# Kernel tuning notes

Measured on AMD Instinct MI355X. Metric: run time of the kernel, lower is better.

The kernel has to match this reference:

```python
import jax, jax.numpy as jnp
import numpy as np

B, L, C, D = 4, 128, 1024, 512

def setup_inputs() -> dict:
    key = jax.random.key(0)
    ks = jax.random.split(key, 6)
    scale = 1.0 / np.sqrt(D)
    return {
        "hidden": jax.random.normal(ks[0], (B, L, D), dtype=jnp.float32),
        "ctx": jax.random.normal(ks[1], (B, C, D), dtype=jnp.float32),
        "W": jax.random.normal(ks[2], (D, D), dtype=jnp.float32) * scale,
        "U": jax.random.normal(ks[3], (D, D), dtype=jnp.float32) * scale,
        "U_b": jax.random.normal(ks[4], (D,), dtype=jnp.float32) * scale,
        "V": jax.random.normal(ks[5], (D,), dtype=jnp.float32) * scale,
    }

def reference(hidden, ctx, W, U, U_b, V):
    # Bahdanau additive attention: softmax_j V . tanh(W h_i + U c_j + b)
    wq = jnp.einsum('bld,ed->ble', hidden, W)          # [B, L, D]
    uc = jnp.einsum('bcd,ed->bce', ctx, U) + U_b       # [B, C, D]
    s = jnp.tanh(wq[:, :, None, :] + uc[:, None, :, :])  # [B, L, C, D]
    align = jnp.einsum('blcd,d->blc', s, V)            # [B, L, C]
    return jax.nn.softmax(align, axis=-1)
```

## Files before the change

### kernel.cpp

```cpp
#include <hip/hip_runtime.h>
#include <hip/hip_bf16.h>


#define SCALE2 2.8853900817779268f

typedef _Float16 f16x8 __attribute__((ext_vector_type(8)));
typedef float f32x4 __attribute__((ext_vector_type(4)));

__device__ __forceinline__ void gload16(const void* g, void* l) {
    __builtin_amdgcn_global_load_lds(
        (const __attribute__((address_space(1))) void*)g,
        (__attribute__((address_space(3))) void*)l,
        16, 0, 0);
}

__global__ __launch_bounds__(256) void gemm_mfma(
    const float* __restrict__ hidden, const float* __restrict__ ctx,
    const float* __restrict__ Wmat, const float* __restrict__ Umat,
    const float* __restrict__ U_b,
    float* __restrict__ ewq_t, float* __restrict__ euc_t)
{
    __shared__ __align__(16) _Float16 Xh[2][64][40];
    __shared__ __align__(16) _Float16 Xl[2][64][40];
    __shared__ __align__(16) _Float16 Wh[2][64][40];
    __shared__ __align__(16) _Float16 Wl[2][64][40];

    const int tid  = threadIdx.x;
    const int lane = tid & 63;
    const int w    = tid >> 6;

    const float *X, *Wm, *bias;
    float* Ct;
    int m0, crow0, Mb, bshift;
    {
        int gb = blockIdx.x;
        if (gb < 64) {
            m0 = (gb & 7) * 64; crow0 = (gb >> 3) * 64;
            X = hidden; Wm = Wmat; bias = nullptr; Ct = ewq_t; Mb = 128; bshift = 7;
        } else {
            int g = gb - 64;
            m0 = (g & 7) * 64; crow0 = (g >> 3) * 64;
            X = ctx; Wm = Umat; bias = U_b; Ct = euc_t; Mb = 1024; bshift = 10;
        }
    }

    const int sr = tid >> 2;
    const int sk = (tid & 3) * 8;
    const float* xsrc = X  + (size_t)(crow0 + sr) * 512 + sk;
    const float* wsrc = Wm + (size_t)(m0    + sr) * 512 + sk;

    f32x4 acc[4];
#pragma unroll
    for (int t = 0; t < 4; ++t) acc[t] = (f32x4){0.f, 0.f, 0.f, 0.f};

    float xr[8], wr[8];
    {
        float4 a = *(const float4*)(xsrc);
        float4 b = *(const float4*)(xsrc + 4);
        float4 c = *(const float4*)(wsrc);
        float4 d = *(const float4*)(wsrc + 4);
        xr[0]=a.x; xr[1]=a.y; xr[2]=a.z; xr[3]=a.w; xr[4]=b.x; xr[5]=b.y; xr[6]=b.z; xr[7]=b.w;
        wr[0]=c.x; wr[1]=c.y; wr[2]=c.z; wr[3]=c.w; wr[4]=d.x; wr[5]=d.y; wr[6]=d.z; wr[7]=d.w;
        f16x8 xh, xl, wh, wl;
#pragma unroll
        for (int i = 0; i < 8; ++i) {
            xh[i] = (_Float16)xr[i]; xl[i] = (_Float16)(xr[i] - (float)xh[i]);
            wh[i] = (_Float16)wr[i]; wl[i] = (_Float16)(wr[i] - (float)wh[i]);
        }
        *(f16x8*)&Xh[0][sr][sk] = xh; *(f16x8*)&Xl[0][sr][sk] = xl;
        *(f16x8*)&Wh[0][sr][sk] = wh; *(f16x8*)&Wl[0][sr][sk] = wl;
    }

    const int fr = lane & 15;
    const int fk = (lane >> 4) * 8;
    const int mrow = w * 16 + fr;

    for (int kc = 0; kc < 16; ++kc) {
        if (kc < 15) {
            float4 a = *(const float4*)(xsrc + (kc + 1) * 32);
            float4 b = *(const float4*)(xsrc + (kc + 1) * 32 + 4);
            float4 c = *(const float4*)(wsrc + (kc + 1) * 32);
            float4 d = *(const float4*)(wsrc + (kc + 1) * 32 + 4);
            xr[0]=a.x; xr[1]=a.y; xr[2]=a.z; xr[3]=a.w; xr[4]=b.x; xr[5]=b.y; xr[6]=b.z; xr[7]=b.w;
            wr[0]=c.x; wr[1]=c.y; wr[2]=c.z; wr[3]=c.w; wr[4]=d.x; wr[5]=d.y; wr[6]=d.z; wr[7]=d.w;
        }
        __syncthreads();
        const int bu = kc & 1;
        const f16x8 ah = *(const f16x8*)&Wh[bu][mrow][fk];
        const f16x8 al = *(const f16x8*)&Wl[bu][mrow][fk];
#pragma unroll
        for (int t = 0; t < 4; ++t) {
            const f16x8 bh = *(const f16x8*)&Xh[bu][t * 16 + fr][fk];
            const f16x8 bl = *(const f16x8*)&Xl[bu][t * 16 + fr][fk];
            acc[t] = __builtin_amdgcn_mfma_f32_16x16x32_f16(ah, bh, acc[t], 0, 0, 0);
            acc[t] = __builtin_amdgcn_mfma_f32_16x16x32_f16(ah, bl, acc[t], 0, 0, 0);
            acc[t] = __builtin_amdgcn_mfma_f32_16x16x32_f16(al, bh, acc[t], 0, 0, 0);
        }
        if (kc < 15) {
            f16x8 xh, xl, wh, wl;
#pragma unroll
            for (int i = 0; i < 8; ++i) {
                xh[i] = (_Float16)xr[i]; xl[i] = (_Float16)(xr[i] - (float)xh[i]);
                wh[i] = (_Float16)wr[i]; wl[i] = (_Float16)(wr[i] - (float)wh[i]);
            }
            *(f16x8*)&Xh[bu ^ 1][sr][sk] = xh; *(f16x8*)&Xl[bu ^ 1][sr][sk] = xl;
            *(f16x8*)&Wh[bu ^ 1][sr][sk] = wh; *(f16x8*)&Wl[bu ^ 1][sr][sk] = wl;
        }
    }

    const int rbase = m0 + w * 16 + (lane >> 4) * 4;
    float bl4[4] = {0.f, 0.f, 0.f, 0.f};
    if (bias) {
        float4 t = *(const float4*)&bias[rbase];
        bl4[0] = t.x; bl4[1] = t.y; bl4[2] = t.z; bl4[3] = t.w;
    }
    const int bidx = crow0 >> bshift;
    const int cl0  = crow0 & (Mb - 1);
    float* obase = Ct + ((size_t)bidx * 512 + rbase) * Mb + cl0 + fr;
#pragma unroll
    for (int r = 0; r < 4; ++r)
#pragma unroll
        for (int t = 0; t < 4; ++t)
            obase[(size_t)r * Mb + t * 16] =
                __builtin_amdgcn_exp2f(SCALE2 * (acc[t][r] + bl4[r]));
}

__global__ __launch_bounds__(256) void fused_align9(
    const float* __restrict__ ewq_t,
    const float* __restrict__ euc_t,
    const float* __restrict__ Vv,
    float* __restrict__ p0, float* __restrict__ p1,
    float* __restrict__ p2, float* __restrict__ p3)
{
    __shared__ __align__(16) float uc_s[2][16][256];
    __shared__ __align__(16) float wq_s[2][16][16];
    __shared__ __align__(8)  float2 v2_s[64];

    const int tid  = threadIdx.x;
    const int lane = tid & 63;
    const int w    = __builtin_amdgcn_readfirstlane(tid >> 6);
    const int c0   = blockIdx.x * 256;
    const int l0   = blockIdx.y * 16;
    const int z    = blockIdx.z;
    const int b    = z >> 2, h = z & 3;
    const int d0   = h * 128;

    const float* ucb = euc_t + ((size_t)b * 512 + d0) * 1024 + c0;
    const float* wqb = ewq_t + ((size_t)b * 512 + d0) * 128 + l0;

    if (tid < 64)
        v2_s[tid] = make_float2(Vv[d0 + 2 * tid], Vv[d0 + 2 * tid + 1]);

#define STAGE(buf, chunk)                                                     \
    {                                                                         \
        _Pragma("unroll")                                                     \
        for (int i_ = 0; i_ < 4; ++i_) {                                      \
            const int d_ = w * 4 + i_;                                        \
            gload16(ucb + (size_t)((chunk) * 16 + d_) * 1024 + lane * 4,      \
                    &uc_s[buf][d_][0]);                                       \
        }                                                                     \
        if (w == 0)                                                           \
            gload16(wqb + (size_t)((chunk) * 16 + (lane >> 2)) * 128 +        \
                        (lane & 3) * 4,                                       \
                    &wq_s[buf][0][0]);                                        \
    }

    float acc[4][4];
#pragma unroll
    for (int i = 0; i < 4; ++i)
#pragma unroll
        for (int k = 0; k < 4; ++k) acc[i][k] = 0.0f;

    STAGE(0, 0);
    __syncthreads();

    for (int ch = 0; ch < 8; ++ch) {
        if (ch < 7) STAGE((ch + 1) & 1, ch + 1);
        const int bu = ch & 1;
#pragma unroll
        for (int j = 0; j < 8; ++j) {
            const float4 e0 = *(const float4*)&uc_s[bu][2 * j][lane * 4];
            const float4 e1 = *(const float4*)&uc_s[bu][2 * j + 1][lane * 4];
            const float4 q0 = *(const float4*)&wq_s[bu][2 * j][w * 4];
            const float4 q1 = *(const float4*)&wq_s[bu][2 * j + 1][w * 4];
            const float2 vp = v2_s[ch * 8 + j];
            const float q0a[4] = {q0.x, q0.y, q0.z, q0.w};
            const float q1a[4] = {q1.x, q1.y, q1.z, q1.w};
            const float e0a[4] = {e0.x, e0.y, e0.z, e0.w};
            const float e1a[4] = {e1.x, e1.y, e1.z, e1.w};
#pragma unroll
            for (int i = 0; i < 4; ++i) {
#pragma unroll
                for (int k = 0; k < 4; ++k) {
                    const float t0 = fmaf(q0a[i], e0a[k], 1.0f);
                    const float t1 = fmaf(q1a[i], e1a[k], 1.0f);
                    const float n  = fmaf(vp.x, t1, vp.y * t0);
                    acc[i][k] = fmaf(n, __builtin_amdgcn_rcpf(t0 * t1), acc[i][k]);
                }
            }
        }
        __syncthreads();
    }
#undef STAGE

    float* pp = (h == 0) ? p0 : (h == 1) ? p1 : (h == 2) ? p2 : p3;
#pragma unroll
    for (int i = 0; i < 4; ++i) {
        float4 r;
        r.x = -2.0f * acc[i][0]; r.y = -2.0f * acc[i][1];
        r.z = -2.0f * acc[i][2]; r.w = -2.0f * acc[i][3];
        *(float4*)(pp + ((size_t)b * 128 + l0 + w * 4 + i) * 1024 + c0 + lane * 4) = r;
    }
}

__global__ __launch_bounds__(256) void softmax3(
    float* __restrict__ data, const float* __restrict__ p1,
    const float* __restrict__ p2, const float* __restrict__ p3)
{
    const int row  = blockIdx.x * 4 + (threadIdx.x >> 6);
    const int lane = threadIdx.x & 63;
    float* p = data + (size_t)row * 1024;
    const float* q1 = p1 + (size_t)row * 1024;
    const float* q2 = p2 + (size_t)row * 1024;
    const float* q3 = p3 + (size_t)row * 1024;

    float4 x[4];
#pragma unroll
    for (int j = 0; j < 4; ++j) {
        float4 a = *(const float4*)(p  + j * 256 + lane * 4);
        float4 b = *(const float4*)(q1 + j * 256 + lane * 4);
        float4 c = *(const float4*)(q2 + j * 256 + lane * 4);
        float4 d = *(const float4*)(q3 + j * 256 + lane * 4);
        x[j].x = (a.x + b.x) + (c.x + d.x);
        x[j].y = (a.y + b.y) + (c.y + d.y);
        x[j].z = (a.z + b.z) + (c.z + d.z);
        x[j].w = (a.w + b.w) + (c.w + d.w);
    }

    float m = x[0].x;
#pragma unroll
    for (int j = 0; j < 4; ++j) {
        m = fmaxf(m, x[j].x); m = fmaxf(m, x[j].y);
        m = fmaxf(m, x[j].z); m = fmaxf(m, x[j].w);
    }
#pragma unroll
    for (int mask = 32; mask >= 1; mask >>= 1) m = fmaxf(m, __shfl_xor(m, mask, 64));

    const float LOG2E = 1.4426950408889634f;
    float s = 0.0f;
#pragma unroll
    for (int j = 0; j < 4; ++j) {
        x[j].x = __builtin_amdgcn_exp2f((x[j].x - m) * LOG2E);
        x[j].y = __builtin_amdgcn_exp2f((x[j].y - m) * LOG2E);
        x[j].z = __builtin_amdgcn_exp2f((x[j].z - m) * LOG2E);
        x[j].w = __builtin_amdgcn_exp2f((x[j].w - m) * LOG2E);
        s += x[j].x + x[j].y + x[j].z + x[j].w;
    }
#pragma unroll
    for (int mask = 32; mask >= 1; mask >>= 1) s += __shfl_xor(s, mask, 64);
    const float r = __builtin_amdgcn_rcpf(s);
#pragma unroll
    for (int j = 0; j < 4; ++j) {
        x[j].x *= r; x[j].y *= r; x[j].z *= r; x[j].w *= r;
        *(float4*)(p + j * 256 + lane * 4) = x[j];
    }
}

extern "C" void kernel_launch(void* const* d_in, const int* in_sizes, int n_in,
                              void* d_out, int out_size, void* d_ws, size_t ws_size,
                              hipStream_t stream)
{
    const float* hidden = (const float*)d_in[0];
    const float* ctx    = (const float*)d_in[1];
    const float* W      = (const float*)d_in[2];
    const float* U      = (const float*)d_in[3];
    const float* U_b    = (const float*)d_in[4];
    const float* V      = (const float*)d_in[5];
    float* out = (float*)d_out;

    float* ewq_t = (float*)d_ws;
    float* euc_t = ewq_t + 4 * 512 * 128;
    float* p1    = euc_t + 4 * 512 * 1024;
    float* p2    = p1 + 4 * 128 * 1024;
    float* p3    = p2 + 4 * 128 * 1024;

    gemm_mfma<<<576, 256, 0, stream>>>(hidden, ctx, W, U, U_b, ewq_t, euc_t);
    fused_align9<<<dim3(4, 8, 16), 256, 0, stream>>>(ewq_t, euc_t, V, out, p1, p2, p3);
    softmax3<<<128, 256, 0, stream>>>(out, p1, p2, p3);
}
```

Measured before the change: 54.27 us.

## Combine 16 rational terms into one fraction per chunk and split D into eight slices

Result: faster. 51.81 us (-4.5%).

```diff
diff --git a/kernel.cpp b/kernel.cpp
--- a/kernel.cpp
+++ b/kernel.cpp
@@ -3,6 +3,7 @@
 
 
 #define SCALE2 2.8853900817779268f
+#define PART (4 * 128 * 1024)
 
 typedef _Float16 f16x8 __attribute__((ext_vector_type(8)));
 typedef float f32x4 __attribute__((ext_vector_type(4)));
@@ -125,16 +126,15 @@
                 __builtin_amdgcn_exp2f(SCALE2 * (acc[t][r] + bl4[r]));
 }
 
-__global__ __launch_bounds__(256) void fused_align9(
+__global__ __launch_bounds__(256) void fused_align10(
     const float* __restrict__ ewq_t,
     const float* __restrict__ euc_t,
     const float* __restrict__ Vv,
-    float* __restrict__ p0, float* __restrict__ p1,
-    float* __restrict__ p2, float* __restrict__ p3)
+    float* __restrict__ pout, float* __restrict__ pws)
 {
     __shared__ __align__(16) float uc_s[2][16][256];
     __shared__ __align__(16) float wq_s[2][16][16];
-    __shared__ __align__(8)  float2 v2_s[64];
+    __shared__ float v_s[64];
 
     const int tid  = threadIdx.x;
     const int lane = tid & 63;
@@ -142,14 +142,13 @@
     const int c0   = blockIdx.x * 256;
     const int l0   = blockIdx.y * 16;
     const int z    = blockIdx.z;
-    const int b    = z >> 2, h = z & 3;
-    const int d0   = h * 128;
+    const int b    = z >> 3, h = z & 7;
+    const int d0   = h * 64;
 
     const float* ucb = euc_t + ((size_t)b * 512 + d0) * 1024 + c0;
     const float* wqb = ewq_t + ((size_t)b * 512 + d0) * 128 + l0;
 
-    if (tid < 64)
-        v2_s[tid] = make_float2(Vv[d0 + 2 * tid], Vv[d0 + 2 * tid + 1]);
+    if (tid < 64) v_s[tid] = Vv[d0 + tid];
 
 #define STAGE(buf, chunk)                                                     \
     {                                                                         \
@@ -171,39 +170,68 @@
 #pragma unroll
         for (int k = 0; k < 4; ++k) acc[i][k] = 0.0f;
 
+#define COMPUTE(bu, ch)                                                       \
+    do {                                                                      \
+        float vr[16];                                                         \
+        _Pragma("unroll")                                                     \
+        for (int j_ = 0; j_ < 4; ++j_) {                                      \
+            const float4 v4_ = *(const float4*)&v_s[(ch) * 16 + j_ * 4];      \
+            vr[j_ * 4 + 0] = v4_.x; vr[j_ * 4 + 1] = v4_.y;                   \
+            vr[j_ * 4 + 2] = v4_.z; vr[j_ * 4 + 3] = v4_.w;                   \
+        }                                                                     \
+        float nn[4][4], dn[4][4];                                             \
+        {                                                                     \
+            const float4 e = *(const float4*)&uc_s[bu][0][lane * 4];          \
+            const float4 q = *(const float4*)&wq_s[bu][0][w * 4];             \
+            const float ea[4] = {e.x, e.y, e.z, e.w};                         \
+            const float qa[4] = {q.x, q.y, q.z, q.w};                         \
+            _Pragma("unroll")                                                 \
+            for (int i = 0; i < 4; ++i)                                       \
+                _Pragma("unroll")                                             \
+                for (int k = 0; k < 4; ++k) {                                 \
+                    dn[i][k] = fmaf(qa[i], ea[k], 1.0f);                      \
+                    nn[i][k] = vr[0];                                         \
+                }                                                             \
+        }                                                                     \
+        _Pragma("unroll")                                                     \
+        for (int dd = 1; dd < 16; ++dd) {                                     \
+            const float4 e = *(const float4*)&uc_s[bu][dd][lane * 4];         \
+            const float4 q = *(const float4*)&wq_s[bu][dd][w * 4];            \
+            const float ea[4] = {e.x, e.y, e.z, e.w};                         \
+            const float qa[4] = {q.x, q.y, q.z, q.w};                         \
+            const float vv = vr[dd];                                          \
+            _Pragma("unroll")                                                 \
+            for (int i = 0; i < 4; ++i)                                       \
+                _Pragma("unroll")                                             \
+                for (int k = 0; k < 4; ++k) {                                 \
+                    const float t_ = fmaf(qa[i], ea[k], 1.0f);                \
+                    nn[i][k] = fmaf(nn[i][k], t_, vv * dn[i][k]);             \
+                    dn[i][k] *= t_;                                           \
+                }                                                             \
+        }                                                                     \
+        _Pragma("unroll")                                                     \
+        for (int i = 0; i < 4; ++i)                                           \
+            _Pragma("unroll")                                                 \
+            for (int k = 0; k < 4; ++k)                                       \
+                acc[i][k] = fmaf(nn[i][k],                                    \
+                                 __builtin_amdgcn_rcpf(dn[i][k]), acc[i][k]); \
+    } while (0)
+
     STAGE(0, 0);
     __syncthreads();
 
-    for (int ch = 0; ch < 8; ++ch) {
-        if (ch < 7) STAGE((ch + 1) & 1, ch + 1);
-        const int bu = ch & 1;
-#pragma unroll
-        for (int j = 0; j < 8; ++j) {
-            const float4 e0 = *(const float4*)&uc_s[bu][2 * j][lane * 4];
-            const float4 e1 = *(const float4*)&uc_s[bu][2 * j + 1][lane * 4];
-            const float4 q0 = *(const float4*)&wq_s[bu][2 * j][w * 4];
-            const float4 q1 = *(const float4*)&wq_s[bu][2 * j + 1][w * 4];
-            const float2 vp = v2_s[ch * 8 + j];
-            const float q0a[4] = {q0.x, q0.y, q0.z, q0.w};
-            const float q1a[4] = {q1.x, q1.y, q1.z, q1.w};
-            const float e0a[4] = {e0.x, e0.y, e0.z, e0.w};
-            const float e1a[4] = {e1.x, e1.y, e1.z, e1.w};
-#pragma unroll
-            for (int i = 0; i < 4; ++i) {
-#pragma unroll
-                for (int k = 0; k < 4; ++k) {
-                    const float t0 = fmaf(q0a[i], e0a[k], 1.0f);
-                    const float t1 = fmaf(q1a[i], e1a[k], 1.0f);
-                    const float n  = fmaf(vp.x, t1, vp.y * t0);
-                    acc[i][k] = fmaf(n, __builtin_amdgcn_rcpf(t0 * t1), acc[i][k]);
-                }
-            }
-        }
+    for (int cc = 0; cc < 2; ++cc) {
+        STAGE(1, 2 * cc + 1);
+        COMPUTE(0, 2 * cc);
         __syncthreads();
+        if (cc == 0) STAGE(0, 2);
+        COMPUTE(1, 2 * cc + 1);
+        __syncthreads();
     }
 #undef STAGE
-
-    float* pp = (h == 0) ? p0 : (h == 1) ? p1 : (h == 2) ? p2 : p3;
+#undef COMPUTE
+
+    float* pp = (h == 0) ? pout : pws + (size_t)(h - 1) * PART;
 #pragma unroll
     for (int i = 0; i < 4; ++i) {
         float4 r;
@@ -213,28 +241,24 @@
     }
 }
 
-__global__ __launch_bounds__(256) void softmax3(
-    float* __restrict__ data, const float* __restrict__ p1,
-    const float* __restrict__ p2, const float* __restrict__ p3)
+__global__ __launch_bounds__(256) void softmax4(
+    float* __restrict__ data, const float* __restrict__ pws)
 {
     const int row  = blockIdx.x * 4 + (threadIdx.x >> 6);
     const int lane = threadIdx.x & 63;
     float* p = data + (size_t)row * 1024;
-    const float* q1 = p1 + (size_t)row * 1024;
-    const float* q2 = p2 + (size_t)row * 1024;
-    const float* q3 = p3 + (size_t)row * 1024;
 
     float4 x[4];
 #pragma unroll
-    for (int j = 0; j < 4; ++j) {
-        float4 a = *(const float4*)(p  + j * 256 + lane * 4);
-        float4 b = *(const float4*)(q1 + j * 256 + lane * 4);
-        float4 c = *(const float4*)(q2 + j * 256 + lane * 4);
-        float4 d = *(const float4*)(q3 + j * 256 + lane * 4);
-        x[j].x = (a.x + b.x) + (c.x + d.x);
-        x[j].y = (a.y + b.y) + (c.y + d.y);
-        x[j].z = (a.z + b.z) + (c.z + d.z);
-        x[j].w = (a.w + b.w) + (c.w + d.w);
+    for (int j = 0; j < 4; ++j) x[j] = *(const float4*)(p + j * 256 + lane * 4);
+#pragma unroll
+    for (int t = 0; t < 7; ++t) {
+        const float* q = pws + (size_t)t * PART + (size_t)row * 1024;
+#pragma unroll
+        for (int j = 0; j < 4; ++j) {
+            const float4 a = *(const float4*)(q + j * 256 + lane * 4);
+            x[j].x += a.x; x[j].y += a.y; x[j].z += a.z; x[j].w += a.w;
+        }
     }
 
     float m = x[0].x;
@@ -280,11 +304,9 @@
 
     float* ewq_t = (float*)d_ws;
     float* euc_t = ewq_t + 4 * 512 * 128;
-    float* p1    = euc_t + 4 * 512 * 1024;
-    float* p2    = p1 + 4 * 128 * 1024;
-    float* p3    = p2 + 4 * 128 * 1024;
+    float* pws   = euc_t + 4 * 512 * 1024;
 
     gemm_mfma<<<576, 256, 0, stream>>>(hidden, ctx, W, U, U_b, ewq_t, euc_t);
-    fused_align9<<<dim3(4, 8, 16), 256, 0, stream>>>(ewq_t, euc_t, V, out, p1, p2, p3);
-    softmax3<<<128, 256, 0, stream>>>(out, p1, p2, p3);
-}
+    fused_align10<<<dim3(4, 8, 32), 256, 0, stream>>>(ewq_t, euc_t, V, out, pws);
+    softmax4<<<128, 256, 0, stream>>>(out, pws);
+}
```
